# Performance work log

Measured on AMD Instinct MI355X. Metric: run time of the kernel, lower is better.

The kernel has to match this reference:

```python
import jax, jax.numpy as jnp
import numpy as np

D_MODEL = 1024
N_HEADS = 16
D_HEAD = D_MODEL // N_HEADS


def setup_inputs() -> dict:
    key = jax.random.key(0)
    k1, k2, k3 = jax.random.split(key, 3)
    x = jax.random.normal(k1, (2, 2048, D_MODEL), dtype=jnp.float32)
    # Dense layer params (glorot-ish scale)
    W_qkv = jax.random.normal(k2, (D_MODEL, 3 * D_MODEL), dtype=jnp.float32) * (1.0 / np.sqrt(D_MODEL))
    b_qkv = jnp.zeros((3 * D_MODEL,), dtype=jnp.float32)
    W_proj = jax.random.normal(k3, (D_MODEL, D_MODEL), dtype=jnp.float32) * (1.0 / np.sqrt(D_MODEL))
    b_proj = jnp.zeros((D_MODEL,), dtype=jnp.float32)
    return {"x": x, "W_qkv": W_qkv, "b_qkv": b_qkv, "W_proj": W_proj, "b_proj": b_proj}


def reference(x, W_qkv, b_qkv, W_proj, b_proj):
    B, S, _ = x.shape
    qkv = x @ W_qkv + b_qkv                      # [B,S,3D]
    q, k, v = jnp.split(qkv, 3, axis=-1)
    # [B,S,D] -> [B,H,S,Dh]
    def to_heads(t):
        return t.reshape(B, S, N_HEADS, D_HEAD).transpose(0, 2, 1, 3)
    q, k, v = to_heads(q), to_heads(k), to_heads(v)
    scores = jnp.einsum('bhqd,bhkd->bhqk', q, k)  # [B,H,S,S]
    causal = jnp.tril(jnp.ones((S, S), dtype=bool))
    # NOTE: mask applied BEFORE scaling, matching the original module.
    scores = jnp.where(causal[None, None, :, :], scores, jnp.float32(-1e9))
    scaled = scores / jnp.sqrt(jnp.float32(D_HEAD))
    attn = jax.nn.softmax(scaled, axis=-1)
    ctx = jnp.einsum('bhqk,bhkd->bhqd', attn, v)  # [B,H,S,Dh]
    ctx = ctx.transpose(0, 2, 1, 3).reshape(B, S, D_MODEL)
    return ctx @ W_proj + b_proj
```

## Files before the change

### kernel.cpp

```cpp
#include <hip/hip_runtime.h>
#include <stdint.h>

typedef __attribute__((ext_vector_type(8))) short short8;
typedef __attribute__((ext_vector_type(4))) float f32x4;

#define QSCALE 0.18033688011112043f

__device__ __forceinline__ unsigned short f2b(float f) {
  union { float f; uint32_t u; } v; v.f = f;
  uint32_t u = v.u;
  u = u + 0x7fffu + ((u >> 16) & 1u);
  return (unsigned short)(u >> 16);
}
__device__ __forceinline__ unsigned int cvtpk(float lo, float hi) {
  unsigned int r;
  asm("v_cvt_pk_bf16_f32 %0, %1, %2" : "=v"(r) : "v"(lo), "v"(hi));
  return r;
}
__device__ __forceinline__ void gload16(const void* g, void* lds) {
  __builtin_amdgcn_global_load_lds((const __attribute__((address_space(1))) void*)g,
                                   (__attribute__((address_space(3))) void*)lds, 16, 0, 0);
}

__global__ __launch_bounds__(256) void cvt_f32_bf16(const float* __restrict__ in,
                                                    unsigned short* __restrict__ out, int n) {
  int i = (blockIdx.x * 256 + threadIdx.x) * 4;
  if (i < n) {
    float4 v = *(const float4*)(in + i);
    ushort4 o;
    o.x = f2b(v.x); o.y = f2b(v.y); o.z = f2b(v.z); o.w = f2b(v.w);
    *(ushort4*)(out + i) = o;
  }
}

__global__ __launch_bounds__(256) void transposeW(const float* __restrict__ W,
                                                  unsigned short* __restrict__ Wt,
                                                  int K, int N, float scale, int scaleRows) {
  __shared__ float tile[32][33];
  int x0 = blockIdx.x * 32, y0 = blockIdx.y * 32;
  int tx = threadIdx.x, ty = threadIdx.y;
  #pragma unroll
  for (int j = 0; j < 4; ++j)
    tile[ty + j * 8][tx] = W[(size_t)(y0 + ty + j * 8) * N + x0 + tx];
  __syncthreads();
  #pragma unroll
  for (int j = 0; j < 4; ++j) {
    int orow = x0 + ty + j * 8;
    float s = (orow < scaleRows) ? scale : 1.0f;
    Wt[(size_t)orow * K + y0 + tx] = f2b(tile[tx][ty + j * 8] * s);
  }
}

template<bool OUTF32>
__global__ __launch_bounds__(256) void gemm_bt(const unsigned short* __restrict__ A,
                                               const unsigned short* __restrict__ Bt,
                                               const float* __restrict__ bias,
                                               void* __restrict__ outp,
                                               int M, int N, int K,
                                               float bscale, int bscaleN, int mtiles) {
  __shared__ unsigned short As[128 * 64];
  __shared__ unsigned short Bs[128 * 64];
  const int t = threadIdx.x;
  const int lane = t & 63;
  const int w = t >> 6;
  const int wm = w >> 1, wn = w & 1;

  const int cpx = gridDim.x >> 3;
  const int swz = (blockIdx.x & 7) * cpx + (blockIdx.x >> 3);
  const int m0 = (swz % mtiles) * 128;
  const int n0 = (swz / mtiles) * 128;

  const f32x4 zero = {0.f, 0.f, 0.f, 0.f};
  f32x4 acc[4][4];
  #pragma unroll
  for (int i = 0; i < 4; ++i)
    #pragma unroll
    for (int j = 0; j < 4; ++j) acc[i][j] = zero;

  const int cl = lane & 15, g = lane >> 4;
  const int srow = t >> 3;
  const int sch  = (t & 7) ^ (srow & 7);

  char* AsB = (char*)As;
  char* BsB = (char*)Bs;

  for (int k0 = 0; k0 < K; k0 += 64) {
    __syncthreads();
    #pragma unroll
    for (int r = 0; r < 4; ++r) {
      int row = r * 32 + srow;
      gload16(A  + (size_t)(m0 + row) * K + k0 + sch * 8, AsB + r * 4096 + t * 16);
      gload16(Bt + (size_t)(n0 + row) * K + k0 + sch * 8, BsB + r * 4096 + t * 16);
    }
    __syncthreads();
    #pragma unroll
    for (int kk = 0; kk < 2; ++kk) {
      short8 af[4], bfr[4];
      #pragma unroll
      for (int f = 0; f < 4; ++f) {
        int arow = wm * 64 + f * 16 + cl;
        int brow = wn * 64 + f * 16 + cl;
        af[f]  = *(const short8*)(AsB + ((arow * 128 + kk * 64 + g * 16) ^ ((cl & 7) << 4)));
        bfr[f] = *(const short8*)(BsB + ((brow * 128 + kk * 64 + g * 16) ^ ((cl & 7) << 4)));
      }
      __builtin_amdgcn_s_setprio(1);
      #pragma unroll
      for (int fm = 0; fm < 4; ++fm)
        #pragma unroll
        for (int fn = 0; fn < 4; ++fn)
          acc[fm][fn] = __builtin_amdgcn_mfma_f32_16x16x32_bf16(af[fm], bfr[fn], acc[fm][fn], 0, 0, 0);
      __builtin_amdgcn_s_setprio(0);
    }
  }

  #pragma unroll
  for (int fn = 0; fn < 4; ++fn) {
    int col = n0 + wn * 64 + fn * 16 + cl;
    float bv = bias[col] * ((col < bscaleN) ? bscale : 1.0f);
    #pragma unroll
    for (int fm = 0; fm < 4; ++fm) {
      int rbase = m0 + wm * 64 + fm * 16 + g * 4;
      #pragma unroll
      for (int r = 0; r < 4; ++r) {
        float vout = acc[fm][fn][r] + bv;
        if (OUTF32) ((float*)outp)[(size_t)(rbase + r) * N + col] = vout;
        else ((unsigned short*)outp)[(size_t)(rbase + r) * N + col] = f2b(vout);
      }
    }
  }
}

__global__ __launch_bounds__(256) void transposeV(const unsigned short* __restrict__ qkv,
                                                  unsigned short* __restrict__ Vt) {
  __shared__ unsigned short tile[64][72];
  const int bh = blockIdx.y, b = bh >> 4, h = bh & 15;
  const int s0 = blockIdx.x * 64;
  const int t = threadIdx.x;
  #pragma unroll
  for (int i = 0; i < 2; ++i) {
    int c = t + i * 256;
    int srow = c >> 3, d0 = (c & 7) * 8;
    short8 v = *(const short8*)(qkv + (size_t)(b * 2048 + s0 + srow) * 3072 + 2048 + h * 64 + d0);
    *(short8*)(&tile[srow][d0]) = v;
  }
  __syncthreads();
  #pragma unroll
  for (int i = 0; i < 2; ++i) {
    int c = t + i * 256;
    int d = c >> 3, sb = (c & 7) * 8;
    short8 o;
    #pragma unroll
    for (int j = 0; j < 8; ++j) o[j] = tile[sb + j][d];
    *(short8*)(Vt + (size_t)(bh * 64 + d) * 2048 + s0 + sb) = o;
  }
}

__device__ __forceinline__ void attn_tile(const short8 ak[4][2], const short8 av[4][2],
                                          const short8 a5[2], const short8 bq[2],
                                          char* Pbuf, f32x4 o[4], f32x4& o5,
                                          float& m, bool maskIter, int cl, int g, int w) {
  f32x4 st[4];
  #pragma unroll
  for (int tt = 0; tt < 4; ++tt) st[tt] = (f32x4){0.f, 0.f, 0.f, 0.f};
  __builtin_amdgcn_s_setprio(1);
  #pragma unroll
  for (int kk = 0; kk < 2; ++kk)
    #pragma unroll
    for (int tt = 0; tt < 4; ++tt)
      st[tt] = __builtin_amdgcn_mfma_f32_16x16x32_bf16(ak[tt][kk], bq[kk], st[tt], 0, 0, 0);
  __builtin_amdgcn_s_setprio(0);

  float z[4][4];
  #pragma unroll
  for (int tt = 0; tt < 4; ++tt)
    #pragma unroll
    for (int r = 0; r < 4; ++r) z[tt][r] = st[tt][r];
  if (maskIter) {
    int q_loc = w * 16 + cl;
    #pragma unroll
    for (int tt = 0; tt < 4; ++tt)
      #pragma unroll
      for (int r = 0; r < 4; ++r)
        if (tt * 16 + 4 * g + r > q_loc) z[tt][r] = -1e30f;
  }
  float cm = z[0][0];
  #pragma unroll
  for (int tt = 0; tt < 4; ++tt)
    #pragma unroll
    for (int r = 0; r < 4; ++r) cm = fmaxf(cm, z[tt][r]);
  cm = fmaxf(cm, __shfl_xor(cm, 16));
  cm = fmaxf(cm, __shfl_xor(cm, 32));

  if (!__all(cm <= m + 8.f)) {
    float mn = fmaxf(m, cm);
    float alpha = exp2f(m - mn);
    m = mn;
    #pragma unroll
    for (int c = 0; c < 4; ++c)
      #pragma unroll
      for (int r = 0; r < 4; ++r) o[c][r] *= alpha;
    o5[0] *= alpha;
  }

  #pragma unroll
  for (int tt = 0; tt < 4; ++tt) {
    float p0 = exp2f(z[tt][0] - m), p1 = exp2f(z[tt][1] - m);
    float p2 = exp2f(z[tt][2] - m), p3 = exp2f(z[tt][3] - m);
    uint2 val;
    val.x = cvtpk(p0, p1);
    val.y = cvtpk(p2, p3);
    *(uint2*)(Pbuf + ((cl * 128 + tt * 32 + g * 8) ^ ((cl & 7) << 4))) = val;
  }
  short8 bp[2];
  #pragma unroll
  for (int kk = 0; kk < 2; ++kk)
    bp[kk] = *(const short8*)(Pbuf + ((cl * 128 + kk * 64 + g * 16) ^ ((cl & 7) << 4)));

  __builtin_amdgcn_s_setprio(1);
  #pragma unroll
  for (int kk = 0; kk < 2; ++kk) {
    #pragma unroll
    for (int c = 0; c < 4; ++c)
      o[c] = __builtin_amdgcn_mfma_f32_16x16x32_bf16(av[c][kk], bp[kk], o[c], 0, 0, 0);
    o5 = __builtin_amdgcn_mfma_f32_16x16x32_bf16(a5[kk], bp[kk], o5, 0, 0, 0);
  }
  __builtin_amdgcn_s_setprio(0);
}

__global__ __launch_bounds__(256, 2) void attn_mfma2(const unsigned short* __restrict__ qkv,
                                                     const unsigned short* __restrict__ Vt,
                                                     unsigned short* __restrict__ ctx) {
  const int p  = blockIdx.x;
  const int bh = blockIdx.y;
  const int b = bh >> 4, h = bh & 15;
  const int qtA = p, qtB = 31 - p;
  const int t = threadIdx.x;
  const int l = t & 63;
  const int w = t >> 6;
  const int cl = l & 15;
  const int g  = l >> 4;

  __shared__ unsigned short Ks[64 * 64];
  __shared__ unsigned short Vs[64 * 64];
  __shared__ unsigned short Ps[4][2][16 * 64];
  __shared__ unsigned short Ones[16 * 64];

  char* KsB = (char*)Ks;
  char* VsB = (char*)Vs;
  char* PbA = (char*)(&Ps[w][0][0]);
  char* PbB = (char*)(&Ps[w][1][0]);
  char* OnB = (char*)Ones;

  {
    int row = t >> 4;
    int c4  = (t & 15) * 4;
    unsigned short vv = (row == 0) ? (unsigned short)0x3F80 : (unsigned short)0;
    ushort4 ov = {vv, vv, vv, vv};
    *(ushort4*)(OnB + ((row * 128 + c4 * 2) ^ ((row & 7) << 4))) = ov;
  }
  __syncthreads();
  short8 a5[2];
  #pragma unroll
  for (int kk = 0; kk < 2; ++kk)
    a5[kk] = *(const short8*)(OnB + ((cl * 128 + kk * 64 + g * 16) ^ ((cl & 7) << 4)));

  const size_t kbase  = (size_t)(b * 2048) * 3072 + 1024 + h * 64;
  const size_t vtbase = (size_t)(bh * 64) * 2048;

  short8 bqA[2], bqB[2];
  {
    const unsigned short* qa = qkv + (size_t)(b * 2048 + qtA * 64 + w * 16 + cl) * 3072 + h * 64 + g * 8;
    bqA[0] = *(const short8*)(qa);
    bqA[1] = *(const short8*)(qa + 32);
    const unsigned short* qb = qkv + (size_t)(b * 2048 + qtB * 64 + w * 16 + cl) * 3072 + h * 64 + g * 8;
    bqB[0] = *(const short8*)(qb);
    bqB[1] = *(const short8*)(qb + 32);
  }

  f32x4 oA[4], oB[4], o5A, o5B;
  #pragma unroll
  for (int c = 0; c < 4; ++c) { oA[c] = (f32x4){0.f,0.f,0.f,0.f}; oB[c] = (f32x4){0.f,0.f,0.f,0.f}; }
  o5A = (f32x4){0.f,0.f,0.f,0.f};
  o5B = (f32x4){0.f,0.f,0.f,0.f};
  float mA = -1e30f, mB = -1e30f;

  for (int jt = 0; jt <= qtB; ++jt) {
    __syncthreads();
    #pragma unroll
    for (int i = 0; i < 2; ++i) {
      int row = i * 32 + w * 8 + (l >> 3);
      int ch  = (l & 7) ^ (l >> 3);
      gload16(qkv + kbase + (size_t)(jt * 64 + row) * 3072 + ch * 8,
              KsB + i * 4096 + w * 1024);
      gload16(Vt + vtbase + (size_t)row * 2048 + jt * 64 + ch * 8,
              VsB + i * 4096 + w * 1024);
    }
    __syncthreads();

    short8 ak[4][2];
    #pragma unroll
    for (int tt = 0; tt < 4; ++tt)
      #pragma unroll
      for (int kk = 0; kk < 2; ++kk)
        ak[tt][kk] = *(const short8*)(KsB + (((tt * 16 + cl) * 128 + kk * 64 + g * 16) ^ ((cl & 7) << 4)));
    short8 av[4][2];
    #pragma unroll
    for (int c = 0; c < 4; ++c)
      #pragma unroll
      for (int kk = 0; kk < 2; ++kk)
        av[c][kk] = *(const short8*)(VsB + (((c * 16 + cl) * 128 + kk * 64 + g * 16) ^ ((cl & 7) << 4)));

    if (jt <= qtA) attn_tile(ak, av, a5, bqA, PbA, oA, o5A, mA, jt == qtA, cl, g, w);
    attn_tile(ak, av, a5, bqB, PbB, oB, o5B, mB, jt == qtB, cl, g, w);
  }

  {
    float lsum = __shfl(o5A[0], cl);
    float inv = 1.f / lsum;
    unsigned short* crow = ctx + (size_t)(b * 2048 + qtA * 64 + w * 16 + cl) * 1024 + h * 64 + g * 4;
    #pragma unroll
    for (int c = 0; c < 4; ++c) {
      uint2 val;
      val.x = cvtpk(oA[c][0] * inv, oA[c][1] * inv);
      val.y = cvtpk(oA[c][2] * inv, oA[c][3] * inv);
      *(uint2*)(crow + c * 16) = val;
    }
  }
  {
    float lsum = __shfl(o5B[0], cl);
    float inv = 1.f / lsum;
    unsigned short* crow = ctx + (size_t)(b * 2048 + qtB * 64 + w * 16 + cl) * 1024 + h * 64 + g * 4;
    #pragma unroll
    for (int c = 0; c < 4; ++c) {
      uint2 val;
      val.x = cvtpk(oB[c][0] * inv, oB[c][1] * inv);
      val.y = cvtpk(oB[c][2] * inv, oB[c][3] * inv);
      *(uint2*)(crow + c * 16) = val;
    }
  }
}

extern "C" void kernel_launch(void* const* d_in, const int* in_sizes, int n_in,
                              void* d_out, int out_size, void* d_ws, size_t ws_size,
                              hipStream_t stream) {
  const float* x     = (const float*)d_in[0];
  const float* Wqkv  = (const float*)d_in[1];
  const float* bqkv  = (const float*)d_in[2];
  const float* Wproj = (const float*)d_in[3];
  const float* bproj = (const float*)d_in[4];
  float* out = (float*)d_out;

  char* ws = (char*)d_ws;
  unsigned short* xb     = (unsigned short*)(ws);
  unsigned short* wqkvT  = (unsigned short*)(ws + 8388608);
  unsigned short* wprojT = (unsigned short*)(ws + 14680064);
  unsigned short* qkv    = (unsigned short*)(ws + 16777216);
  unsigned short* ctx    = (unsigned short*)(ws + 41943040);
  unsigned short* vt     = (unsigned short*)(ws + 50331648);

  cvt_f32_bf16<<<4096, 256, 0, stream>>>(x, xb, 4096 * 1024);

  dim3 tb(32, 8);
  transposeW<<<dim3(3072 / 32, 1024 / 32), tb, 0, stream>>>(Wqkv, wqkvT, 1024, 3072, QSCALE, 1024);
  transposeW<<<dim3(1024 / 32, 1024 / 32), tb, 0, stream>>>(Wproj, wprojT, 1024, 1024, 1.0f, 0);

  gemm_bt<false><<<768, 256, 0, stream>>>(xb, wqkvT, bqkv, qkv, 4096, 3072, 1024,
                                          QSCALE, 1024, 32);

  transposeV<<<dim3(32, 32), 256, 0, stream>>>(qkv, vt);

  attn_mfma2<<<dim3(16, 32), 256, 0, stream>>>(qkv, vt, ctx);

  gemm_bt<true><<<256, 256, 0, stream>>>(ctx, wprojT, bproj, out, 4096, 1024, 1024,
                                         1.0f, 0, 32);
}
```

Baseline: 212.5 us.

## Double-buffer LDS tiles in GEMM and attention kernels to prefetch next tile

Both the bf16 GEMM and the causal attention kernel now keep two LDS buffers. The next K-slice (GEMM) or K/V tile (attention) is issued with asynchronous global-to-LDS loads before the MFMA work on the current buffer. Each loop now has one barrier at the end of the iteration instead of two per step, so global load latency can overlap with compute. The GEMM also drops the s_setprio bracketing. In exchange, LDS use per block doubles for the GEMM tiles and grows for attention, which may lower occupancy.

```diff
diff --git a/kernel.cpp b/kernel.cpp
--- a/kernel.cpp
+++ b/kernel.cpp
@@ -58,8 +58,8 @@
                                                void* __restrict__ outp,
                                                int M, int N, int K,
                                                float bscale, int bscaleN, int mtiles) {
-  __shared__ unsigned short As[128 * 64];
-  __shared__ unsigned short Bs[128 * 64];
+  __shared__ unsigned short As[2][128 * 64];
+  __shared__ unsigned short Bs[2][128 * 64];
   const int t = threadIdx.x;
   const int lane = t & 63;
   const int w = t >> 6;
@@ -81,18 +81,24 @@
   const int srow = t >> 3;
   const int sch  = (t & 7) ^ (srow & 7);
 
-  char* AsB = (char*)As;
-  char* BsB = (char*)Bs;
-
-  for (int k0 = 0; k0 < K; k0 += 64) {
-    __syncthreads();
+  auto stage = [&](int k0, int buf) {
     #pragma unroll
     for (int r = 0; r < 4; ++r) {
       int row = r * 32 + srow;
-      gload16(A  + (size_t)(m0 + row) * K + k0 + sch * 8, AsB + r * 4096 + t * 16);
-      gload16(Bt + (size_t)(n0 + row) * K + k0 + sch * 8, BsB + r * 4096 + t * 16);
-    }
-    __syncthreads();
+      gload16(A  + (size_t)(m0 + row) * K + k0 + sch * 8, (char*)As[buf] + r * 4096 + t * 16);
+      gload16(Bt + (size_t)(n0 + row) * K + k0 + sch * 8, (char*)Bs[buf] + r * 4096 + t * 16);
+    }
+  };
+
+  stage(0, 0);
+  __syncthreads();
+
+  const int nk = K >> 6;
+  for (int ki = 0; ki < nk; ++ki) {
+    const int cur = ki & 1;
+    if (ki + 1 < nk) stage((ki + 1) << 6, cur ^ 1);
+    char* AsB = (char*)As[cur];
+    char* BsB = (char*)Bs[cur];
     #pragma unroll
     for (int kk = 0; kk < 2; ++kk) {
       short8 af[4], bfr[4];
@@ -103,14 +109,13 @@
         af[f]  = *(const short8*)(AsB + ((arow * 128 + kk * 64 + g * 16) ^ ((cl & 7) << 4)));
         bfr[f] = *(const short8*)(BsB + ((brow * 128 + kk * 64 + g * 16) ^ ((cl & 7) << 4)));
       }
-      __builtin_amdgcn_s_setprio(1);
       #pragma unroll
       for (int fm = 0; fm < 4; ++fm)
         #pragma unroll
         for (int fn = 0; fn < 4; ++fn)
           acc[fm][fn] = __builtin_amdgcn_mfma_f32_16x16x32_bf16(af[fm], bfr[fn], acc[fm][fn], 0, 0, 0);
-      __builtin_amdgcn_s_setprio(0);
-    }
+    }
+    __syncthreads();
   }
 
   #pragma unroll
@@ -240,16 +245,29 @@
   const int cl = l & 15;
   const int g  = l >> 4;
 
-  __shared__ unsigned short Ks[64 * 64];
-  __shared__ unsigned short Vs[64 * 64];
+  __shared__ unsigned short Ks[2][64 * 64];
+  __shared__ unsigned short Vs[2][64 * 64];
   __shared__ unsigned short Ps[4][2][16 * 64];
   __shared__ unsigned short Ones[16 * 64];
 
-  char* KsB = (char*)Ks;
-  char* VsB = (char*)Vs;
   char* PbA = (char*)(&Ps[w][0][0]);
   char* PbB = (char*)(&Ps[w][1][0]);
   char* OnB = (char*)Ones;
+
+  const size_t kbase  = (size_t)(b * 2048) * 3072 + 1024 + h * 64;
+  const size_t vtbase = (size_t)(bh * 64) * 2048;
+
+  auto stage = [&](int jt, int buf) {
+    #pragma unroll
+    for (int i = 0; i < 2; ++i) {
+      int row = i * 32 + w * 8 + (l >> 3);
+      int ch  = (l & 7) ^ (l >> 3);
+      gload16(qkv + kbase + (size_t)(jt * 64 + row) * 3072 + ch * 8,
+              (char*)Ks[buf] + i * 4096 + w * 1024);
+      gload16(Vt + vtbase + (size_t)row * 2048 + jt * 64 + ch * 8,
+              (char*)Vs[buf] + i * 4096 + w * 1024);
+    }
+  };
 
   {
     int row = t >> 4;
@@ -258,14 +276,14 @@
     ushort4 ov = {vv, vv, vv, vv};
     *(ushort4*)(OnB + ((row * 128 + c4 * 2) ^ ((row & 7) << 4))) = ov;
   }
+
+  stage(0, 0);
   __syncthreads();
+
   short8 a5[2];
   #pragma unroll
   for (int kk = 0; kk < 2; ++kk)
     a5[kk] = *(const short8*)(OnB + ((cl * 128 + kk * 64 + g * 16) ^ ((cl & 7) << 4)));
-
-  const size_t kbase  = (size_t)(b * 2048) * 3072 + 1024 + h * 64;
-  const size_t vtbase = (size_t)(bh * 64) * 2048;
 
   short8 bqA[2], bqB[2];
   {
@@ -285,17 +303,10 @@
   float mA = -1e30f, mB = -1e30f;
 
   for (int jt = 0; jt <= qtB; ++jt) {
-    __syncthreads();
-    #pragma unroll
-    for (int i = 0; i < 2; ++i) {
-      int row = i * 32 + w * 8 + (l >> 3);
-      int ch  = (l & 7) ^ (l >> 3);
-      gload16(qkv + kbase + (size_t)(jt * 64 + row) * 3072 + ch * 8,
-              KsB + i * 4096 + w * 1024);
-      gload16(Vt + vtbase + (size_t)row * 2048 + jt * 64 + ch * 8,
-              VsB + i * 4096 + w * 1024);
-    }
-    __syncthreads();
+    const int cur = jt & 1;
+    if (jt < qtB) stage(jt + 1, cur ^ 1);
+    char* KsB = (char*)Ks[cur];
+    char* VsB = (char*)Vs[cur];
 
     short8 ak[4][2];
     #pragma unroll
@@ -312,6 +323,8 @@
 
     if (jt <= qtA) attn_tile(ak, av, a5, bqA, PbA, oA, o5A, mA, jt == qtA, cl, g, w);
     attn_tile(ak, av, a5, bqB, PbB, oB, o5B, mB, jt == qtB, cl, g, w);
+
+    __syncthreads();
   }
 
   {
```

New measurement: 197.7 us. -7.0%, faster.
